# Kernel optimization log

Measured on AMD Instinct MI355X. Metric: run time of the kernel, lower is better.

## Reference

```python
import jax, jax.numpy as jnp
import numpy as np

B, L, C_IN = 32, 1024, 21
D, H, DFF, MODES, LAYERS = 512, 8, 2048, 64, 2
E = D // H            # 64, matches FourierBlock weights1 [8, D//8, D//8, modes]
K_MA = 25             # moving_avg kernel
EPS = 1e-5

def _pos_encoding(n, d):
    pos = np.arange(n)[:, None].astype(np.float32)
    div = np.exp(np.arange(0, d, 2).astype(np.float32) * -(np.log(10000.0) / d))
    pe = np.zeros((n, d), np.float32)
    pe[:, 0::2] = np.sin(pos * div)
    pe[:, 1::2] = np.cos(pos * div)
    return jnp.asarray(pe)

PE = _pos_encoding(L, D)

def _moving_avg(x, k):
    # series_decomp: replicate-pad (k-1)//2 on both ends, then mean window k
    pad = (k - 1) // 2
    xp = jnp.pad(x, ((0, 0), (pad, pad), (0, 0)), mode='edge')
    return jax.lax.reduce_window(xp, 0.0, jax.lax.add, (1, k, 1), (1, 1, 1), 'VALID') / k

def _layernorm(x, g, b):
    mu = x.mean(-1, keepdims=True)
    var = ((x - mu) ** 2).mean(-1, keepdims=True)
    return (x - mu) * jax.lax.rsqrt(var + EPS) * g + b

def _fourier_block(q, w_cplx):
    # q: [B,L,H,E] -> [B,H,E,L]; keep only lowest MODES frequencies,
    # complex per-mode channel mixing, then inverse rFFT.
    x = q.transpose(0, 2, 3, 1)
    x_ft = jnp.fft.rfft(x, axis=-1)                          # [B,H,E,L//2+1] complex
    out_m = jnp.einsum('bhem,heom->bhom', x_ft[..., :MODES], w_cplx)
    out_ft = jnp.zeros(x_ft.shape[:3] + (L // 2 + 1,), jnp.complex64)
    out_ft = out_ft.at[..., :MODES].set(out_m)
    return jnp.fft.irfft(out_ft, n=L, axis=-1)               # [B,H,E,L] real

def _forward(x_enc, conv_w, wq, bq, wo, bo, fw_re, fw_im, conv1_w, conv2_w,
             enc_g, enc_b, ff_w, ff_b, ffn_g, ffn_b, reg_w, reg_b):
    # DataEmbedding_onlypos: circular Conv1d(k=3, no bias) + sinusoidal PE (dropout=0)
    xt = x_enc.transpose(0, 2, 1)                            # [B,C,L]
    xp = jnp.pad(xt, ((0, 0), (0, 0), (1, 1)), mode='wrap')
    emb = jax.lax.conv_general_dilated(xp, conv_w, (1,), 'VALID',
                                       dimension_numbers=('NCH', 'OIH', 'NCH'))
    x = emb.transpose(0, 2, 1) + PE                          # [B,L,D]
    for l in range(LAYERS):
        # AutoCorrelationLayer: only the query projection feeds FourierBlock
        q = (jnp.einsum('bld,kd->blk', x, wq[l]) + bq[l]).reshape(B, L, H, E)
        new_x = _fourier_block(q, fw_re[l] + 1j * fw_im[l])  # [B,H,E,L]
        # torch .view(B, L, -1) on contiguous [B,H,E,L] = raw reshape
        new_x = new_x.reshape(B, L, H * E)
        new_x = jnp.einsum('bld,kd->blk', new_x, wo[l]) + bo[l]
        x = x + new_x
        x = x - _moving_avg(x, K_MA)                         # decomp1 -> residual part
        y = jax.nn.gelu(jnp.einsum('bld,fd->blf', x, conv1_w[l]), approximate=False)
        y = jnp.einsum('blf,df->bld', y, conv2_w[l])
        xy = x + y
        x = xy - _moving_avg(xy, K_MA)                       # decomp2 -> residual part
    # my_Layernorm: LN then subtract per-sequence mean
    x = _layernorm(x, enc_g, enc_b)
    x = x - x.mean(axis=1, keepdims=True)
    x = _layernorm(jnp.einsum('bld,kd->blk', x, ff_w) + ff_b, ffn_g, ffn_b)
    flat = x.reshape(B, L * D)
    return flat @ reg_w.T + reg_b                            # [B,1]

def setup_inputs():
    key = jax.random.key(0)
    ks = jax.random.split(key, 12)
    r = lambda k, shp, s=0.02: jax.random.normal(k, shp, jnp.float32) * s
    scale = 1.0 / (D * D)
    return {
        'x_enc': jax.random.normal(ks[0], (B, L, C_IN), jnp.float32),
        'conv_w': r(ks[1], (D, C_IN, 3), 0.05),
        'wq': r(ks[2], (LAYERS, D, D)),
        'bq': jnp.zeros((LAYERS, D), jnp.float32),
        'wo': r(ks[3], (LAYERS, D, D)),
        'bo': jnp.zeros((LAYERS, D), jnp.float32),
        'fw_re': jax.random.uniform(ks[4], (LAYERS, H, E, E, MODES), jnp.float32) * scale,
        'fw_im': jax.random.uniform(ks[5], (LAYERS, H, E, E, MODES), jnp.float32) * scale,
        'conv1_w': r(ks[6], (LAYERS, DFF, D)),
        'conv2_w': r(ks[7], (LAYERS, D, DFF)),
        'enc_g': jnp.ones((D,), jnp.float32),
        'enc_b': jnp.zeros((D,), jnp.float32),
        'ff_w': r(ks[8], (D, D)),
        'ff_b': jnp.zeros((D,), jnp.float32),
        'ffn_g': jnp.ones((D,), jnp.float32),
        'ffn_b': jnp.zeros((D,), jnp.float32),
        'reg_w': r(ks[9], (1, D * L)),
        'reg_b': jnp.zeros((1,), jnp.float32),
    }

def reference(x_enc, conv_w, wq, bq, wo, bo, fw_re, fw_im, conv1_w, conv2_w,
              enc_g, enc_b, ff_w, ff_b, ffn_g, ffn_b, reg_w, reg_b):
    return _forward(x_enc, conv_w, wq, bq, wo, bo, fw_re, fw_im, conv1_w, conv2_w,
                    enc_g, enc_b, ff_w, ff_b, ffn_g, ffn_b, reg_w, reg_b)
```

## Files before the change

kernel.cpp:

```cpp
#include <hip/hip_runtime.h>
#include <math.h>

static constexpr int B_   = 32;
static constexpr int L_   = 1024;
static constexpr int CIN_ = 21;
static constexpr int D_   = 512;
static constexpr int H_   = 8;
static constexpr int E_   = 64;
static constexpr int DFF_ = 2048;
static constexpr int M_   = 64;

typedef unsigned short u16;
typedef __attribute__((ext_vector_type(8))) short bf16x8;
typedef __attribute__((ext_vector_type(4))) float f32x4;
typedef __attribute__((ext_vector_type(4))) unsigned short u16x4;

static __device__ __forceinline__ u16 f2b(float f) {
    unsigned u = __float_as_uint(f);
    unsigned r = (u + 0x7fffu + ((u >> 16) & 1u)) >> 16;
    return (u16)r;
}
static __device__ __forceinline__ float b2f(u16 x) {
    return __uint_as_float((unsigned)x << 16);
}

static __device__ __forceinline__ void gload16(const u16* g, u16* l) {
    unsigned long long ga = (unsigned long long)g;
    unsigned la = (unsigned)(unsigned long long)l;
    __builtin_amdgcn_global_load_lds(
        (const __attribute__((address_space(1))) void*)ga,
        (__attribute__((address_space(3))) void*)(unsigned long long)la,
        16, 0, 0);
}

__global__ void k_tables(u16* trig, u16* tcat, float* pe) {
    int idx = blockIdx.x * 256 + threadIdx.x;
    if (idx < 131072) {
        int l = idx & 1023, mc = idx >> 10;
        int m = mc & 63;
        float th = (float)((m * l) & 1023) * 0.006135923151542565f;
        float v = (mc < 64) ? cosf(th) : (-sinf(th));
        trig[idx] = f2b(v);
    }
    if (idx < 131072) {
        int k = idx & 127, l = idx >> 7;
        int m = k & 63;
        float th = (float)((m * l) & 1023) * 0.006135923151542565f;
        float v;
        if (k < 64) v = (m == 0) ? 1.0f : (2.0f * cosf(th));
        else        v = (m == 0) ? 0.0f : (-2.0f * sinf(th));
        tcat[idx] = f2b(v * (1.0f / 1024.0f));
    }
    if (idx < 524288) {
        int d = idx & 511, l = idx >> 9;
        int i2 = d >> 1;
        float div = expf(-(float)(2 * i2) * 0.017988946039015984f);
        float arg = (float)l * div;
        pe[idx] = (d & 1) ? cosf(arg) : sinf(arg);
    }
}

__global__ void k_cast(const float* __restrict__ in, u16* __restrict__ out, int n4) {
    int i = blockIdx.x * 256 + threadIdx.x;
    if (i < n4) {
        float4 v = ((const float4*)in)[i];
        u16x4 o = { f2b(v.x), f2b(v.y), f2b(v.z), f2b(v.w) };
        ((u16x4*)out)[i] = o;
    }
}

__global__ void k_wtrans(const float* __restrict__ re, const float* __restrict__ im,
                         u16* __restrict__ outre, u16* __restrict__ outim) {
    __shared__ float t[64][65];
    const float* src = blockIdx.z ? im : re;
    u16* dst = blockIdx.z ? outim : outre;
    int h = blockIdx.y, eo0 = blockIdx.x * 64;
    int j = threadIdx.x & 63, i0 = threadIdx.x >> 6;
    for (int i = i0; i < 64; i += 4)
        t[i][j] = src[(size_t)h * 262144 + (size_t)(eo0 + i) * 64 + j];
    __syncthreads();
    for (int i = i0; i < 64; i += 4)
        dst[(size_t)h * 262144 + (size_t)i * 4096 + eo0 + j] = f2b(t[j][i]);
}

__global__ void k_im2col(const float* __restrict__ xe, u16* __restrict__ a2) {
    int idx = blockIdx.x * 256 + threadIdx.x;
    int row = idx >> 4, g = idx & 15;
    int b = row >> 10, l = row & 1023;
    u16x4 o;
    #pragma unroll
    for (int j = 0; j < 4; ++j) {
        int kc = g * 4 + j;
        float v = 0.f;
        if (kc < 63) {
            int c = kc / 3, k = kc - c * 3;
            int ls = (l + k - 1 + 1024) & 1023;
            v = xe[((size_t)b * 1024 + ls) * 21 + c];
        }
        o[j] = f2b(v);
    }
    *(u16x4*)(a2 + (size_t)row * 64 + g * 4) = o;
}

__global__ void k_wpad(const float* __restrict__ cw, u16* __restrict__ w2) {
    int idx = blockIdx.x * 256 + threadIdx.x;
    int d = idx >> 6, kc = idx & 63;
    float v = (kc < 63) ? cw[(size_t)d * 63 + kc] : 0.f;
    w2[idx] = f2b(v);
}

template<bool BIAS, bool BIASR, bool GELU, bool ADD, bool WF32, bool WBF16,
         bool DFTZ = false, bool PEADD = false>
__global__ __launch_bounds__(256, 3) void k_mfma(
        const u16* __restrict__ A, const u16* __restrict__ W,
        const float* __restrict__ bias, const float* addp,
        float* C32, u16* C16,
        int K, int lda, int ldw, int ldc, long strideA, long strideC) {
    __shared__ __align__(16) u16 As0[128 * 32];
    __shared__ __align__(16) u16 As1[128 * 32];
    __shared__ __align__(16) u16 Bs0[128 * 32];
    __shared__ __align__(16) u16 Bs1[128 * 32];
    const int tid  = threadIdx.x;
    const int lane = tid & 63, wid = tid >> 6;
    int m0, n0;
    size_t cbase;
    if constexpr (DFTZ) {
        int z  = blockIdx.z;
        int ks = z >> 5;
        m0 = 0;
        n0 = blockIdx.x * 128;
        A += (size_t)ks * 256;
        W += (size_t)(z & 31) * 1024 + (size_t)ks * 256;
        cbase = (size_t)z * 65536;
    } else {
        int gx = gridDim.x;
        int nwg = gx * gridDim.y;
        int lid = blockIdx.y * gx + blockIdx.x;
        int logical = (lid & 7) * (nwg >> 3) + (lid >> 3);
        m0 = (logical / gx) * 128;
        n0 = (logical % gx) * 128;
        A += (size_t)blockIdx.z * strideA;
        cbase = (size_t)blockIdx.z * strideC;
    }

    const int srow = lane >> 2, scol = (lane & 3) * 8;
    const u16* ga0 = A + (size_t)(m0 + wid * 32 + srow) * lda + scol;
    const u16* ga1 = ga0 + (size_t)16 * lda;
    const u16* gb0 = W + (size_t)(n0 + wid * 32 + srow) * ldw + scol;
    const u16* gb1 = gb0 + (size_t)16 * ldw;
    const int lofs0 = wid * 32 * 32, lofs1 = lofs0 + 16 * 32;

    const int wr = wid >> 1, wc = wid & 1;
    const int fr = lane & 15, fg = lane >> 4;

    f32x4 acc[4][4];
    #pragma unroll
    for (int i = 0; i < 4; ++i)
        #pragma unroll
        for (int j = 0; j < 4; ++j)
            acc[i][j] = f32x4{0.f, 0.f, 0.f, 0.f};

    for (int k0 = 0; k0 < K; k0 += 64) {
        __syncthreads();
        gload16(ga0 + k0,      &As0[lofs0]);
        gload16(ga1 + k0,      &As0[lofs1]);
        gload16(gb0 + k0,      &Bs0[lofs0]);
        gload16(gb1 + k0,      &Bs0[lofs1]);
        gload16(ga0 + k0 + 32, &As1[lofs0]);
        gload16(ga1 + k0 + 32, &As1[lofs1]);
        gload16(gb0 + k0 + 32, &Bs1[lofs0]);
        gload16(gb1 + k0 + 32, &Bs1[lofs1]);
        __syncthreads();
        {
            bf16x8 af[4], bfr[4];
            #pragma unroll
            for (int i = 0; i < 4; ++i) {
                af[i]  = *(const bf16x8*)&As0[(wr * 64 + i * 16 + fr) * 32 + fg * 8];
                bfr[i] = *(const bf16x8*)&Bs0[(wc * 64 + i * 16 + fr) * 32 + fg * 8];
            }
            #pragma unroll
            for (int i = 0; i < 4; ++i)
                #pragma unroll
                for (int j = 0; j < 4; ++j)
                    acc[i][j] = __builtin_amdgcn_mfma_f32_16x16x32_bf16(
                        af[i], bfr[j], acc[i][j], 0, 0, 0);
        }
        {
            bf16x8 af[4], bfr[4];
            #pragma unroll
            for (int i = 0; i < 4; ++i) {
                af[i]  = *(const bf16x8*)&As1[(wr * 64 + i * 16 + fr) * 32 + fg * 8];
                bfr[i] = *(const bf16x8*)&Bs1[(wc * 64 + i * 16 + fr) * 32 + fg * 8];
            }
            #pragma unroll
            for (int i = 0; i < 4; ++i)
                #pragma unroll
                for (int j = 0; j < 4; ++j)
                    acc[i][j] = __builtin_amdgcn_mfma_f32_16x16x32_bf16(
                        af[i], bfr[j], acc[i][j], 0, 0, 0);
        }
    }

    #pragma unroll
    for (int i = 0; i < 4; ++i) {
        #pragma unroll
        for (int j = 0; j < 4; ++j) {
            #pragma unroll
            for (int r = 0; r < 4; ++r) {
                int row = m0 + wr * 64 + i * 16 + fg * 4 + r;
                int col = n0 + wc * 64 + j * 16 + fr;
                float v = acc[i][j][r];
                if (BIAS)  v += bias[col];
                if (BIASR) v += bias[row];
                if (GELU) v = 0.5f * v * (1.f + erff(v * 0.70710678118f));
                size_t o = cbase + (size_t)row * ldc + col;
                if (PEADD) v += addp[(size_t)(row & 1023) * 512 + col];
                if (ADD)   v += addp[o];
                if (WF32) C32[o] = v;
                if (WBF16) C16[o] = f2b(v);
            }
        }
    }
}

__global__ void k_modemix(const float* __restrict__ ftT,
                          const u16* __restrict__ wtre, const u16* __restrict__ wtim,
                          u16* __restrict__ acat) {
    __shared__ float wr_s[64][64];
    __shared__ float wi_s[64][64];
    __shared__ float fr_s[32][64];
    __shared__ float fi_s[32][64];
    int h = blockIdx.x >> 6, m = blockIdx.x & 63;
    int tid = threadIdx.x;
    const u16* wr_p = wtre + ((size_t)(h * 64 + m)) * 4096;
    const u16* wi_p = wtim + ((size_t)(h * 64 + m)) * 4096;
    for (int i = tid; i < 4096; i += 256) {
        wr_s[i >> 6][i & 63] = b2f(wr_p[i]);
        wi_s[i >> 6][i & 63] = b2f(wi_p[i]);
    }
    const size_t KS = (size_t)32 * 65536;
    for (int i = tid; i < 2048; i += 256) {
        int b = i >> 6, e = i & 63;
        size_t f0 = (size_t)b * 65536 + (size_t)m * 512 + h * 64 + e;
        size_t f1 = f0 + (size_t)64 * 512;
        fr_s[b][e] = ftT[f0] + ftT[f0 + KS] + ftT[f0 + 2 * KS] + ftT[f0 + 3 * KS];
        fi_s[b][e] = ftT[f1] + ftT[f1 + KS] + ftT[f1 + 2 * KS] + ftT[f1 + 3 * KS];
    }
    __syncthreads();
    int o = tid & 63, bg = tid >> 6;
    for (int bb = bg; bb < 32; bb += 4) {
        float accr = 0.f, acci = 0.f;
        #pragma unroll 8
        for (int e = 0; e < 64; ++e) {
            float wr = wr_s[e][o], wi = wi_s[e][o];
            float fr = fr_s[bb][e], fi = fi_s[bb][e];
            accr += fr * wr - fi * wi;
            acci += fr * wi + fi * wr;
        }
        size_t base = (((size_t)(bb * 8 + h)) * 64 + o) * 128;
        acat[base + m]      = f2b(accr);
        acat[base + 64 + m] = f2b(acci);
    }
}

__global__ void k_madiff(const float* __restrict__ in, float* __restrict__ out,
                         u16* __restrict__ out16) {
    int b = blockIdx.x, ls = blockIdx.y;
    int d2 = threadIdx.x;
    const float2* base = (const float2*)(in + (size_t)b * 524288) + d2;
    int l0 = ls * 64;
    float sx = 0.f, sy = 0.f;
    #pragma unroll
    for (int k = -12; k <= 12; ++k) {
        int ll = l0 + k;
        ll = ll < 0 ? 0 : (ll > 1023 ? 1023 : ll);
        float2 v = base[(size_t)ll * 256];
        sx += v.x; sy += v.y;
    }
    for (int li = 0; li < 64; ++li) {
        int l = l0 + li;
        float2 x = base[(size_t)l * 256];
        float vx = x.x - sx * (1.f / 25.f);
        float vy = x.y - sy * (1.f / 25.f);
        size_t o = (size_t)b * 262144 + (size_t)l * 256 + d2;
        ((float2*)out)[o] = float2{vx, vy};
        unsigned pk = (unsigned)f2b(vx) | ((unsigned)f2b(vy) << 16);
        ((unsigned*)out16)[o] = pk;
        int lp = l + 13; lp = lp > 1023 ? 1023 : lp;
        int lm = l - 12; lm = lm < 0 ? 0 : lm;
        float2 a = base[(size_t)lp * 256];
        float2 s = base[(size_t)lm * 256];
        sx += a.x - s.x; sy += a.y - s.y;
    }
}

__global__ void k_layernorm(const float* __restrict__ in, const float* __restrict__ g,
                            const float* __restrict__ bta, float* __restrict__ out) {
    int row = blockIdx.x;
    int tid = threadIdx.x;
    const float* r = in + (size_t)row * 512;
    float v0 = r[tid], v1 = r[tid + 256];
    float s = v0 + v1, s2 = v0 * v0 + v1 * v1;
    #pragma unroll
    for (int off = 32; off; off >>= 1) {
        s  += __shfl_down(s, off);
        s2 += __shfl_down(s2, off);
    }
    __shared__ float ws[4], ws2[4];
    if ((tid & 63) == 0) { ws[tid >> 6] = s; ws2[tid >> 6] = s2; }
    __syncthreads();
    if (tid == 0) {
        ws[0]  = ws[0] + ws[1] + ws[2] + ws[3];
        ws2[0] = ws2[0] + ws2[1] + ws2[2] + ws2[3];
    }
    __syncthreads();
    float mu = ws[0] * (1.f / 512.f);
    float var = ws2[0] * (1.f / 512.f) - mu * mu;
    float rs = rsqrtf(var + 1e-5f);
    float* o = out + (size_t)row * 512;
    o[tid]       = (v0 - mu) * rs * g[tid]       + bta[tid];
    o[tid + 256] = (v1 - mu) * rs * g[tid + 256] + bta[tid + 256];
}

__global__ void k_lnreg(const float* __restrict__ in, const float* __restrict__ g,
                        const float* __restrict__ bta, const float* __restrict__ rw,
                        float* __restrict__ partial) {
    int row = blockIdx.x;
    int tid = threadIdx.x;
    const float* r = in + (size_t)row * 512;
    float v0 = r[tid], v1 = r[tid + 256];
    float s = v0 + v1, s2 = v0 * v0 + v1 * v1;
    #pragma unroll
    for (int off = 32; off; off >>= 1) {
        s  += __shfl_down(s, off);
        s2 += __shfl_down(s2, off);
    }
    __shared__ float ws[4], ws2[4];
    if ((tid & 63) == 0) { ws[tid >> 6] = s; ws2[tid >> 6] = s2; }
    __syncthreads();
    if (tid == 0) {
        ws[0]  = ws[0] + ws[1] + ws[2] + ws[3];
        ws2[0] = ws2[0] + ws2[1] + ws2[2] + ws2[3];
    }
    __syncthreads();
    float mu = ws[0] * (1.f / 512.f);
    float var = ws2[0] * (1.f / 512.f) - mu * mu;
    float rs = rsqrtf(var + 1e-5f);
    const float* wrow = rw + (size_t)(row & 1023) * 512;
    float y0 = (v0 - mu) * rs * g[tid]       + bta[tid];
    float y1 = (v1 - mu) * rs * g[tid + 256] + bta[tid + 256];
    float p = y0 * wrow[tid] + y1 * wrow[tid + 256];
    #pragma unroll
    for (int off = 32; off; off >>= 1) p += __shfl_down(p, off);
    __shared__ float wp[4];
    if ((tid & 63) == 0) wp[tid >> 6] = p;
    __syncthreads();
    if (tid == 0) partial[row] = wp[0] + wp[1] + wp[2] + wp[3];
}

__global__ void k_regf2(const float* __restrict__ partial, const float* __restrict__ rb,
                        float* __restrict__ out) {
    int b = blockIdx.x;
    int tid = threadIdx.x;
    const float* p = partial + (size_t)b * 1024;
    float s = p[tid] + p[tid + 256] + p[tid + 512] + p[tid + 768];
    #pragma unroll
    for (int off = 32; off; off >>= 1) s += __shfl_down(s, off);
    __shared__ float ws[4];
    if ((tid & 63) == 0) ws[tid >> 6] = s;
    __syncthreads();
    if (tid == 0) out[b] = ws[0] + ws[1] + ws[2] + ws[3] + rb[0];
}

__global__ __launch_bounds__(512) void k_colmean1(const float* __restrict__ in,
                                                  float* __restrict__ part) {
    int b = blockIdx.x, seg = blockIdx.y;
    int d = threadIdx.x;
    const float* p = in + ((size_t)b * 1024 + seg * 128) * 512 + d;
    float s = 0.f;
    for (int l = 0; l < 128; ++l) s += p[(size_t)l * 512];
    part[((size_t)b * 8 + seg) * 512 + d] = s;
}

__global__ void k_colmean2(const float* __restrict__ part, float* __restrict__ mean) {
    int i = blockIdx.x * 256 + threadIdx.x;
    int b = i >> 9, d = i & 511;
    float s = 0.f;
    #pragma unroll
    for (int seg = 0; seg < 8; ++seg) s += part[((size_t)b * 8 + seg) * 512 + d];
    mean[i] = s * (1.f / 1024.f);
}

__global__ void k_subcol(float* __restrict__ x, const float* __restrict__ mean,
                         u16* __restrict__ x16) {
    int idx = blockIdx.x * 256 + threadIdx.x;
    int d = idx & 511;
    int b = idx >> 19;
    float v = x[idx] - mean[b * 512 + d];
    x[idx] = v;
    x16[idx] = f2b(v);
}

extern "C" void kernel_launch(void* const* d_in, const int* in_sizes, int n_in,
                              void* d_out, int out_size, void* d_ws, size_t ws_size,
                              hipStream_t stream) {
    const float* x_enc  = (const float*)d_in[0];
    const float* conv_w = (const float*)d_in[1];
    const float* wq     = (const float*)d_in[2];
    const float* bq     = (const float*)d_in[3];
    const float* wo     = (const float*)d_in[4];
    const float* bo     = (const float*)d_in[5];
    const float* fw_re  = (const float*)d_in[6];
    const float* fw_im  = (const float*)d_in[7];
    const float* c1w    = (const float*)d_in[8];
    const float* c2w    = (const float*)d_in[9];
    const float* enc_g  = (const float*)d_in[10];
    const float* enc_b  = (const float*)d_in[11];
    const float* ff_w   = (const float*)d_in[12];
    const float* ff_b   = (const float*)d_in[13];
    const float* ffn_g  = (const float*)d_in[14];
    const float* ffn_b  = (const float*)d_in[15];
    const float* reg_w  = (const float*)d_in[16];
    const float* reg_b  = (const float*)d_in[17];
    float* out = (float*)d_out;

    char* wsb = (char*)d_ws;
    float* F0    = (float*)(wsb);
    float* F1    = (float*)(wsb + 67108864);
    u16*   A16   = (u16*)  (wsb + 134217728);
    u16*   U16   = (u16*)  (wsb + 167772160);
    u16*   AC16  = (u16*)  (wsb + 201326592);
    float* FTT   = (float*)(wsb + 205520896);
    float* PE    = (float*)(wsb + 213909504);
    u16*   TRIG  = (u16*)  (wsb + 216006656);
    u16*   TCAT  = (u16*)  (wsb + 216268800);
    u16*   WQ16  = (u16*)  (wsb + 216530944);
    u16*   WO16  = (u16*)  (wsb + 217579520);
    u16*   C1W16 = (u16*)  (wsb + 218628096);
    u16*   C2W16 = (u16*)  (wsb + 222822400);
    u16*   FFW16 = (u16*)  (wsb + 227016704);
    float* CMEAN = (float*)(wsb + 227540992);
    const size_t need_bytes = 227606528;
    if (ws_size < need_bytes) return;

    u16* WTRE16 = (u16*)FTT;
    u16* WTIM16 = WTRE16 + 2097152;

    const int BLD = B_ * L_ * D_;
    dim3 blk(256);

    k_tables<<<2048, blk, 0, stream>>>(TRIG, TCAT, PE);
    k_cast<<<512,  blk, 0, stream>>>(wq,   WQ16,  524288 / 4);
    k_cast<<<512,  blk, 0, stream>>>(wo,   WO16,  524288 / 4);
    k_cast<<<2048, blk, 0, stream>>>(c1w,  C1W16, 2097152 / 4);
    k_cast<<<2048, blk, 0, stream>>>(c2w,  C2W16, 2097152 / 4);
    k_cast<<<256,  blk, 0, stream>>>(ff_w, FFW16, 262144 / 4);
    k_wpad<<<128, blk, 0, stream>>>(conv_w, AC16);
    k_im2col<<<2048, blk, 0, stream>>>(x_enc, U16);
    k_mfma<false, false, false, false, true, true, false, true>
        <<<dim3(4, 256), blk, 0, stream>>>(
        U16, AC16, nullptr, PE, F0, A16, 64, 64, 64, 512, 0, 0);

    float* cur = F0;
    float* alt = F1;
    const dim3 g_big(4, 256);

    for (int l = 0; l < 2; ++l) {
        const float* bq_l = bq + l * 512;
        const float* bo_l = bo + l * 512;
        const u16* wo16_l = WO16 + (size_t)l * 262144;
        const u16* c1_l   = C1W16 + (size_t)l * DFF_ * D_;
        const u16* c2_l   = C2W16 + (size_t)l * D_ * DFF_;
        const float* fwre_l = fw_re + (size_t)l * H_ * E_ * E_ * M_;
        const float* fwim_l = fw_im + (size_t)l * H_ * E_ * E_ * M_;

        k_wtrans<<<dim3(64, 8, 2), blk, 0, stream>>>(fwre_l, fwim_l, WTRE16, WTIM16);
        k_mfma<false, true, false, false, false, true><<<dim3(256, 4), blk, 0, stream>>>(
            WQ16 + (size_t)l * 262144, A16, bq_l, nullptr, nullptr, U16,
            512, 512, 512, 32768, 0, 0);
        float* ftt4 = alt;
        k_mfma<false, false, false, false, true, false, true>
            <<<dim3(4, 1, 128), blk, 0, stream>>>(
            TRIG, U16, nullptr, nullptr, ftt4, nullptr,
            256, 1024, 32768, 512, 0, 0);
        k_modemix<<<512, blk, 0, stream>>>(ftt4, WTRE16, WTIM16, AC16);
        k_mfma<false, false, false, false, false, true><<<dim3(8, 128), blk, 0, stream>>>(
            AC16, TCAT, nullptr, nullptr, nullptr, U16, 128, 128, 128, 1024, 0, 0);
        k_mfma<true, false, false, true, true, false><<<g_big, blk, 0, stream>>>(
            U16, wo16_l, bo_l, cur, cur, nullptr, 512, 512, 512, 512, 0, 0);
        k_madiff<<<dim3(32, 16), blk, 0, stream>>>(cur, alt, A16);
        { float* t = cur; cur = alt; alt = t; }
        u16* y16 = (u16*)alt;
        for (int c = 0; c < 2; ++c) {
            const size_t aoff = (size_t)c * 16384 * 512;
            k_mfma<false, false, true, false, false, true><<<dim3(16, 128), blk, 0, stream>>>(
                A16 + aoff, c1_l, nullptr, nullptr, nullptr, y16,
                512, 512, 512, 2048, 0, 0);
            k_mfma<false, false, false, true, true, false><<<dim3(4, 128), blk, 0, stream>>>(
                y16, c2_l, nullptr, cur + aoff, cur + aoff, nullptr,
                2048, 2048, 2048, 512, 0, 0);
        }
        k_madiff<<<dim3(32, 16), blk, 0, stream>>>(cur, alt, A16);
        { float* t = cur; cur = alt; alt = t; }
    }

    k_layernorm<<<32768, blk, 0, stream>>>(cur, enc_g, enc_b, alt);
    k_colmean1<<<dim3(B_, 8), 512, 0, stream>>>(alt, FTT);
    k_colmean2<<<64, blk, 0, stream>>>(FTT, CMEAN);
    k_subcol<<<BLD / 256, blk, 0, stream>>>(alt, CMEAN, A16);
    k_mfma<true, false, false, false, true, false><<<g_big, blk, 0, stream>>>(
        A16, FFW16, ff_b, nullptr, cur, nullptr, 512, 512, 512, 512, 0, 0);
    k_lnreg<<<32768, blk, 0, stream>>>(cur, ffn_g, ffn_b, reg_w, FTT);
    k_regf2<<<32, blk, 0, stream>>>(FTT, reg_b, out);
}
```

Before: 1.050 ms.

## Software-pipeline GEMM K-loop with double-buffered LDS and async prefetch

Replaces the load-all-then-compute K loop with a two-stage pipeline. LDS holds two 32-wide K slices, and the next-next slice is prefetched while MFMAs run on the current one. Manual vmcnt/lgkmcnt waits and raw s_barrier control the ordering. This hides global-to-LDS latency behind matrix math, at the cost of fragile hand-written wait counts that depend on gload16 issuing exactly one vm op per call.

```diff
diff --git a/kernel.cpp b/kernel.cpp
--- a/kernel.cpp
+++ b/kernel.cpp
@@ -116,10 +116,8 @@
         const float* __restrict__ bias, const float* addp,
         float* C32, u16* C16,
         int K, int lda, int ldw, int ldc, long strideA, long strideC) {
-    __shared__ __align__(16) u16 As0[128 * 32];
-    __shared__ __align__(16) u16 As1[128 * 32];
-    __shared__ __align__(16) u16 Bs0[128 * 32];
-    __shared__ __align__(16) u16 Bs1[128 * 32];
+    __shared__ __align__(16) u16 As[2][128 * 32];
+    __shared__ __align__(16) u16 Bs[2][128 * 32];
     const int tid  = threadIdx.x;
     const int lane = tid & 63, wid = tid >> 6;
     int m0, n0;
@@ -153,6 +151,13 @@
     const int wr = wid >> 1, wc = wid & 1;
     const int fr = lane & 15, fg = lane >> 4;
 
+    auto stagef = [&](int p, int k0) {
+        gload16(ga0 + k0, &As[p][lofs0]);
+        gload16(ga1 + k0, &As[p][lofs1]);
+        gload16(gb0 + k0, &Bs[p][lofs0]);
+        gload16(gb1 + k0, &Bs[p][lofs1]);
+    };
+
     f32x4 acc[4][4];
     #pragma unroll
     for (int i = 0; i < 4; ++i)
@@ -160,45 +165,36 @@
         for (int j = 0; j < 4; ++j)
             acc[i][j] = f32x4{0.f, 0.f, 0.f, 0.f};
 
-    for (int k0 = 0; k0 < K; k0 += 64) {
-        __syncthreads();
-        gload16(ga0 + k0,      &As0[lofs0]);
-        gload16(ga1 + k0,      &As0[lofs1]);
-        gload16(gb0 + k0,      &Bs0[lofs0]);
-        gload16(gb1 + k0,      &Bs0[lofs1]);
-        gload16(ga0 + k0 + 32, &As1[lofs0]);
-        gload16(ga1 + k0 + 32, &As1[lofs1]);
-        gload16(gb0 + k0 + 32, &Bs1[lofs0]);
-        gload16(gb1 + k0 + 32, &Bs1[lofs1]);
-        __syncthreads();
-        {
-            bf16x8 af[4], bfr[4];
+    const int nt = K >> 5;
+    stagef(0, 0);
+    stagef(1, 32);
+
+    for (int t = 0; t < nt; ++t) {
+        const int p = t & 1;
+        if (t < nt - 1) {
+            asm volatile("s_waitcnt vmcnt(4)" ::: "memory");
+        } else {
+            asm volatile("s_waitcnt vmcnt(0)" ::: "memory");
+        }
+        __builtin_amdgcn_sched_barrier(0);
+        __builtin_amdgcn_s_barrier();
+        bf16x8 af[4], bfr[4];
+        #pragma unroll
+        for (int i = 0; i < 4; ++i) {
+            af[i]  = *(const bf16x8*)&As[p][(wr * 64 + i * 16 + fr) * 32 + fg * 8];
+            bfr[i] = *(const bf16x8*)&Bs[p][(wc * 64 + i * 16 + fr) * 32 + fg * 8];
+        }
+        __builtin_amdgcn_sched_barrier(0);
+        asm volatile("s_waitcnt lgkmcnt(0)" ::: "memory");
+        __builtin_amdgcn_sched_barrier(0);
+        __builtin_amdgcn_s_barrier();
+        if (t + 2 < nt) stagef(p, (t + 2) * 32);
+        #pragma unroll
+        for (int i = 0; i < 4; ++i)
             #pragma unroll
-            for (int i = 0; i < 4; ++i) {
-                af[i]  = *(const bf16x8*)&As0[(wr * 64 + i * 16 + fr) * 32 + fg * 8];
-                bfr[i] = *(const bf16x8*)&Bs0[(wc * 64 + i * 16 + fr) * 32 + fg * 8];
-            }
-            #pragma unroll
-            for (int i = 0; i < 4; ++i)
-                #pragma unroll
-                for (int j = 0; j < 4; ++j)
-                    acc[i][j] = __builtin_amdgcn_mfma_f32_16x16x32_bf16(
-                        af[i], bfr[j], acc[i][j], 0, 0, 0);
-        }
-        {
-            bf16x8 af[4], bfr[4];
-            #pragma unroll
-            for (int i = 0; i < 4; ++i) {
-                af[i]  = *(const bf16x8*)&As1[(wr * 64 + i * 16 + fr) * 32 + fg * 8];
-                bfr[i] = *(const bf16x8*)&Bs1[(wc * 64 + i * 16 + fr) * 32 + fg * 8];
-            }
-            #pragma unroll
-            for (int i = 0; i < 4; ++i)
-                #pragma unroll
-                for (int j = 0; j < 4; ++j)
-                    acc[i][j] = __builtin_amdgcn_mfma_f32_16x16x32_bf16(
-                        af[i], bfr[j], acc[i][j], 0, 0, 0);
-        }
+            for (int j = 0; j < 4; ++j)
+                acc[i][j] = __builtin_amdgcn_mfma_f32_16x16x32_bf16(
+                    af[i], bfr[j], acc[i][j], 0, 0, 0);
     }
 
     #pragma unroll
```

Result: no change. 1.070 ms (+1.8%).
